# Performance work log

Measured on AMD Instinct MI355X. Metric: run time of the kernel, lower is better.

The kernel has to match this reference:

```python
import jax, jax.numpy as jnp
import numpy as np

EMBED_DIM = 1024
NUM_HEADS = 16
HEAD_DIM = EMBED_DIM // NUM_HEADS
B, S = 4, 2048


def setup_inputs() -> dict:
    key = jax.random.key(0)
    ks = jax.random.split(key, 9)
    scale = 1.0 / np.sqrt(EMBED_DIM)
    x = jax.random.normal(ks[0], (B, S, EMBED_DIM), dtype=jnp.float32)
    Wq = jax.random.normal(ks[1], (EMBED_DIM, EMBED_DIM), dtype=jnp.float32) * scale
    Wk = jax.random.normal(ks[2], (EMBED_DIM, EMBED_DIM), dtype=jnp.float32) * scale
    Wv = jax.random.normal(ks[3], (EMBED_DIM, EMBED_DIM), dtype=jnp.float32) * scale
    Wo = jax.random.normal(ks[4], (EMBED_DIM, EMBED_DIM), dtype=jnp.float32) * scale
    bq = jnp.zeros((EMBED_DIM,), jnp.float32)
    bk = jnp.zeros((EMBED_DIM,), jnp.float32)
    bv = jnp.zeros((EMBED_DIM,), jnp.float32)
    bo = jnp.zeros((EMBED_DIM,), jnp.float32)
    return {"x": x, "Wq": Wq, "bq": bq, "Wk": Wk, "bk": bk, "Wv": Wv, "bv": bv, "Wo": Wo, "bo": bo}


def _split_heads(t):
    # [B,S,E] -> [B,H,S,D]
    b, s, _ = t.shape
    return t.reshape(b, s, NUM_HEADS, HEAD_DIM).transpose(0, 2, 1, 3)


def reference(x, Wq, bq, Wk, bk, Wv, bv, Wo, bo):
    q = _split_heads(x @ Wq + bq)
    k = _split_heads(x @ Wk + bk)
    v = _split_heads(x @ Wv + bv)
    scale = 1.0 / jnp.sqrt(jnp.asarray(HEAD_DIM, x.dtype))
    scores = jnp.einsum('bhqd,bhkd->bhqk', q, k) * scale  # [B,H,S,S]
    weights = jax.nn.softmax(scores, axis=-1)
    attn = jnp.einsum('bhqk,bhkd->bhqd', weights, v)  # [B,H,S,D]
    b, h, s, d = attn.shape
    concat = attn.transpose(0, 2, 1, 3).reshape(b, s, h * d)
    return concat @ Wo + bo
```

## Files before the change

### kernel.cpp

```cpp
#include <hip/hip_runtime.h>
#include <hip/hip_bf16.h>

typedef unsigned short u16;
typedef __attribute__((ext_vector_type(8))) short bf16x8;
typedef __attribute__((ext_vector_type(4))) float f32x4;
typedef __attribute__((ext_vector_type(4))) unsigned int u32x4;

#define EMB 1024
#define SEQ 2048
#define NH 16
#define HD 64

#define OFF_WT   0u
#define OFF_WOT  3145728u
#define OFF_Q    4194304u
#define OFF_K    12582912u
#define OFF_VT   20971520u
#define OFF_OC   29360128u

#define QSCALE 0.1803368801111f

__device__ __forceinline__ u16 f2bf(float f) {
    unsigned int x; __builtin_memcpy(&x, &f, 4);
    unsigned int r = x + 0x7fffu + ((x >> 16) & 1u);
    return (u16)(r >> 16);
}

#if defined(__has_builtin) && __has_builtin(__builtin_amdgcn_cvt_pk_bf16_f32)
typedef __attribute__((ext_vector_type(2))) __bf16 bfv2;
__device__ __forceinline__ unsigned int pkbf(float a, float b) {
    bfv2 v = __builtin_amdgcn_cvt_pk_bf16_f32(a, b);
    unsigned int u; __builtin_memcpy(&u, &v, 4); return u;
}
#else
__device__ __forceinline__ unsigned int pkbf(float a, float b) {
    return (unsigned)f2bf(a) | ((unsigned)f2bf(b) << 16);
}
#endif

#if defined(__has_builtin) && __has_builtin(__builtin_amdgcn_exp2f)
__device__ __forceinline__ float exp2fast(float x) { return __builtin_amdgcn_exp2f(x); }
#else
__device__ __forceinline__ float exp2fast(float x) { return __builtin_exp2f(x); }
#endif

__device__ __forceinline__ void gld_lds16(const void* gsrc, void* ldst) {
    void* g = const_cast<void*>(gsrc);
    __builtin_amdgcn_global_load_lds((__attribute__((address_space(1))) void*)g,
                                     (__attribute__((address_space(3))) void*)ldst,
                                     16, 0, 0);
}

__global__ __launch_bounds__(256) void convert_x(
    const float* __restrict__ x, u16* __restrict__ xb)
{
    int i = (blockIdx.x * 256 + threadIdx.x) * 4;
    float4 v = *(const float4*)&x[i];
    uint2 o = { pkbf(v.x, v.y), pkbf(v.z, v.w) };
    *(uint2*)&xb[i] = o;
}

__global__ __launch_bounds__(256) void transpose_w(
    const float* __restrict__ W0, const float* __restrict__ W1,
    const float* __restrict__ W2, const float* __restrict__ W3,
    u16* __restrict__ ws)
{
    __shared__ u16 tile[64 * 65];
    const float* src = blockIdx.z == 0 ? W0 : blockIdx.z == 1 ? W1 : blockIdx.z == 2 ? W2 : W3;
    u16* dst = ws + (blockIdx.z < 3 ? (unsigned)blockIdx.z * 1048576u : OFF_WOT);
    const int k0 = blockIdx.x * 64, n0 = blockIdx.y * 64;
    const int t = threadIdx.x;
    #pragma unroll
    for (int i = 0; i < 16; i++) {
        int idx = i * 256 + t; int r = idx >> 6, c = idx & 63;
        tile[c * 65 + r] = f2bf(src[(k0 + r) * EMB + n0 + c]);
    }
    __syncthreads();
    #pragma unroll
    for (int i = 0; i < 16; i++) {
        int idx = i * 256 + t; int r = idx >> 6, c = idx & 63;
        dst[(n0 + r) * EMB + k0 + c] = tile[r * 65 + c];
    }
}

__global__ __launch_bounds__(256) void gemm_qkv(
    const u16* __restrict__ X, const u16* __restrict__ WT,
    const float* __restrict__ bq, const float* __restrict__ bk, const float* __restrict__ bv,
    u16* __restrict__ Qt, u16* __restrict__ Ko, u16* __restrict__ Vt)
{
    __shared__ u16 Al[128 * 32];
    __shared__ u16 Bl[128 * 32];
    const int t = threadIdx.x, lane = t & 63, w = t >> 6;
    const int quad = lane >> 4, l15 = lane & 15;
    const int wr = w >> 1, wc = w & 1;
    const int m0 = blockIdx.x * 128, n0 = blockIdx.y * 128;
    const f32x4 fzero = {0.f, 0.f, 0.f, 0.f};

    f32x4 acc[4][4];
    #pragma unroll
    for (int i = 0; i < 4; i++)
        #pragma unroll
        for (int j = 0; j < 4; j++) acc[i][j] = fzero;

    for (int kt = 0; kt < 32; ++kt) {
        #pragma unroll
        for (int r = 0; r < 2; r++) {
            int g = r * 256 + t; int row = g >> 2, cw = g & 3;
            int sc = (cw ^ ((row >> 1) & 3)) * 8;
            gld_lds16(X  + (size_t)(m0 + row) * EMB + kt * 32 + sc, &Al[g * 8]);
            gld_lds16(WT + (size_t)(n0 + row) * EMB + kt * 32 + sc, &Bl[g * 8]);
        }
        __syncthreads();
        bf16x8 af[4], bfr[4];
        #pragma unroll
        for (int i = 0; i < 4; i++) {
            int rowA = wr * 64 + i * 16 + l15;
            af[i] = *(const bf16x8*)&Al[rowA * 32 + ((quad ^ ((rowA >> 1) & 3)) * 8)];
        }
        #pragma unroll
        for (int j = 0; j < 4; j++) {
            int rowB = wc * 64 + j * 16 + l15;
            bfr[j] = *(const bf16x8*)&Bl[rowB * 32 + ((quad ^ ((rowB >> 1) & 3)) * 8)];
        }
        #pragma unroll
        for (int i = 0; i < 4; i++)
            #pragma unroll
            for (int j = 0; j < 4; j++)
                acc[i][j] = __builtin_amdgcn_mfma_f32_16x16x32_bf16(af[i], bfr[j], acc[i][j], 0, 0, 0);
        __syncthreads();
    }

    const int seg = n0 >> 10;
    const float* bias = seg == 0 ? bq : (seg == 1 ? bk : bv);
    #pragma unroll
    for (int j = 0; j < 4; j++) {
        int n = n0 + wc * 64 + j * 16 + l15;
        int nn = n & 1023;
        float bvl = bias[nn];
        int h = nn >> 6, d = nn & 63;
        #pragma unroll
        for (int i = 0; i < 4; i++) {
            int m = m0 + wr * 64 + i * 16 + quad * 4;
            int b = m >> 11, s = m & 2047;
            if (seg == 0) {
                uint2 pp = { pkbf((acc[i][j][0] + bvl) * QSCALE, (acc[i][j][1] + bvl) * QSCALE),
                             pkbf((acc[i][j][2] + bvl) * QSCALE, (acc[i][j][3] + bvl) * QSCALE) };
                *(uint2*)&Qt[(size_t)((b * NH + h) * HD + d) * SEQ + s] = pp;
            } else if (seg == 2) {
                uint2 pp = { pkbf(acc[i][j][0] + bvl, acc[i][j][1] + bvl),
                             pkbf(acc[i][j][2] + bvl, acc[i][j][3] + bvl) };
                *(uint2*)&Vt[(size_t)((b * NH + h) * HD + d) * SEQ + s] = pp;
            } else {
                size_t base = (size_t)((b * NH + h) * SEQ + s) * HD + d;
                #pragma unroll
                for (int r = 0; r < 4; r++) Ko[base + (size_t)r * HD] = f2bf(acc[i][j][r] + bvl);
            }
        }
    }
}

__global__ __launch_bounds__(256, 2) void flash_attn(
    const u16* __restrict__ Q, const u16* __restrict__ K,
    const u16* __restrict__ VT, u16* __restrict__ Oc)
{
    __shared__ u16 Kl[2][64 * 64];
    __shared__ u16 Vl[2][64 * 64];
    const int t = threadIdx.x, lane = t & 63, w = t >> 6;
    const int quad = lane >> 4, l15 = lane & 15;
    const int a7 = l15 & 7;

    const int lin = blockIdx.x;
    const int xcd = lin & 7, slot = lin >> 3;
    const int bh = xcd * 8 + (slot >> 3);
    const int qx = slot & 7;
    const int b = bh >> 4, h = bh & 15;
    const int q0 = qx * 256 + w * 64;

    const u16* Qtb = Q + (size_t)bh * HD * SEQ;
    const u16* Kb  = K + (size_t)bh * SEQ * HD;
    const u16* Vb  = VT + (size_t)bh * HD * SEQ;
    const f32x4 fzero = {0.f, 0.f, 0.f, 0.f};

    const int kf0 = l15 * 64 + ((quad ^ a7) * 8);
    const int kf1 = l15 * 64 + (((4 + quad) ^ a7) * 8);

    bf16x8 ones;
    #pragma unroll
    for (int j = 0; j < 8; j++) ones[j] = (short)0x3F80;

    bf16x8 qf[4][2];
    #pragma unroll
    for (int i = 0; i < 4; i++)
        #pragma unroll
        for (int c = 0; c < 2; c++)
            #pragma unroll
            for (int j = 0; j < 8; j++)
                qf[i][c][j] = (short)Qtb[(size_t)(c * 32 + quad * 8 + j) * SEQ + q0 + i * 16 + l15];

    f32x4 oacc[4][4];
    f32x4 oextra[4];
    #pragma unroll
    for (int i = 0; i < 4; i++) {
        oextra[i] = fzero;
        #pragma unroll
        for (int f = 0; f < 4; f++) oacc[i][f] = fzero;
    }

    auto stage = [&](int kt, int bsel) {
        #pragma unroll
        for (int r = 0; r < 2; r++) {
            int g = r * 256 + t, row = g >> 3, cw = g & 7;
            int swz = (cw ^ (row & 7)) * 8;
            gld_lds16(Kb + (size_t)kt * 64 * HD + row * HD + swz, &Kl[bsel][g * 8]);
            gld_lds16(Vb + (size_t)row * SEQ + kt * 64 + swz, &Vl[bsel][g * 8]);
        }
    };

    stage(0, 0);
    asm volatile("s_waitcnt vmcnt(0) lgkmcnt(0)" ::: "memory");
    __builtin_amdgcn_s_barrier();
    __builtin_amdgcn_sched_barrier(0);

    int cur = 0;
    for (int kt = 0; kt < 32; ++kt) {
        if (kt < 31) stage(kt + 1, cur ^ 1);

        const u16* kbuf = &Kl[cur][0];
        const u16* vbuf = &Vl[cur][0];
        bf16x8 ak[2][4], av[2][4];
        #pragma unroll
        for (int f = 0; f < 4; f++) {
            ak[0][f] = *(const bf16x8*)(kbuf + kf0 + f * 1024);
            ak[1][f] = *(const bf16x8*)(kbuf + kf1 + f * 1024);
            av[0][f] = *(const bf16x8*)(vbuf + kf0 + f * 1024);
            av[1][f] = *(const bf16x8*)(vbuf + kf1 + f * 1024);
        }

        #pragma unroll
        for (int i = 0; i < 4; i++) {
            f32x4 sf[4];
            #pragma unroll
            for (int f = 0; f < 4; f++) sf[f] = fzero;
            __builtin_amdgcn_s_setprio(1);
            #pragma unroll
            for (int c = 0; c < 2; c++)
                #pragma unroll
                for (int f = 0; f < 4; f++)
                    sf[f] = __builtin_amdgcn_mfma_f32_16x16x32_bf16(ak[c][f], qf[i][c], sf[f], 0, 0, 0);
            __builtin_amdgcn_s_setprio(0);

            unsigned int pa[4][2];
            #pragma unroll
            for (int f = 0; f < 4; f++) {
                pa[f][0] = pkbf(exp2fast(sf[f][0]), exp2fast(sf[f][1]));
                pa[f][1] = pkbf(exp2fast(sf[f][2]), exp2fast(sf[f][3]));
            }

            unsigned int z0 = pa[0][0], w0 = pa[1][0];
            asm("v_permlane32_swap_b32 %0, %1" : "+v"(z0), "+v"(w0));
            asm("v_permlane16_swap_b32 %0, %1" : "+v"(z0), "+v"(w0));
            unsigned int z1 = pa[0][1], w1 = pa[1][1];
            asm("v_permlane32_swap_b32 %0, %1" : "+v"(z1), "+v"(w1));
            asm("v_permlane16_swap_b32 %0, %1" : "+v"(z1), "+v"(w1));
            unsigned int z2 = pa[2][0], w2 = pa[3][0];
            asm("v_permlane32_swap_b32 %0, %1" : "+v"(z2), "+v"(w2));
            asm("v_permlane16_swap_b32 %0, %1" : "+v"(z2), "+v"(w2));
            unsigned int z3 = pa[2][1], w3 = pa[3][1];
            asm("v_permlane32_swap_b32 %0, %1" : "+v"(z3), "+v"(w3));
            asm("v_permlane16_swap_b32 %0, %1" : "+v"(z3), "+v"(w3));

            bf16x8 bp0, bp1;
            { u32x4 u = {z0, z1, w0, w1}; __builtin_memcpy(&bp0, &u, 16); }
            { u32x4 u = {z2, z3, w2, w3}; __builtin_memcpy(&bp1, &u, 16); }

            __builtin_amdgcn_s_setprio(1);
            #pragma unroll
            for (int f = 0; f < 4; f++) {
                oacc[i][f] = __builtin_amdgcn_mfma_f32_16x16x32_bf16(av[0][f], bp0, oacc[i][f], 0, 0, 0);
                oacc[i][f] = __builtin_amdgcn_mfma_f32_16x16x32_bf16(av[1][f], bp1, oacc[i][f], 0, 0, 0);
            }
            oextra[i] = __builtin_amdgcn_mfma_f32_16x16x32_bf16(ones, bp0, oextra[i], 0, 0, 0);
            oextra[i] = __builtin_amdgcn_mfma_f32_16x16x32_bf16(ones, bp1, oextra[i], 0, 0, 0);
            __builtin_amdgcn_s_setprio(0);
        }

        if (kt < 31) {
            asm volatile("s_waitcnt vmcnt(0) lgkmcnt(0)" ::: "memory");
            __builtin_amdgcn_s_barrier();
            __builtin_amdgcn_sched_barrier(0);
        }
        cur ^= 1;
    }

    #pragma unroll
    for (int i = 0; i < 4; i++) {
        float inv = 1.0f / oextra[i][0];
        int s = q0 + i * 16 + l15;
        size_t base = ((size_t)(b * SEQ + s) * NH + h) * HD;
        #pragma unroll
        for (int f = 0; f < 4; f++) {
            uint2 o = { pkbf(oacc[i][f][0] * inv, oacc[i][f][1] * inv),
                        pkbf(oacc[i][f][2] * inv, oacc[i][f][3] * inv) };
            *(uint2*)&Oc[base + f * 16 + quad * 4] = o;
        }
    }
}

__global__ __launch_bounds__(256) void gemm_out(
    const u16* __restrict__ A, const u16* __restrict__ WT,
    const float* __restrict__ bo, float* __restrict__ out)
{
    __shared__ u16 Al[128 * 32];
    __shared__ u16 Bl[128 * 32];
    const int t = threadIdx.x, lane = t & 63, w = t >> 6;
    const int quad = lane >> 4, l15 = lane & 15;
    const int wr = w >> 1, wc = w & 1;
    const int m0 = blockIdx.x * 128, n0 = blockIdx.y * 128;
    const f32x4 fzero = {0.f, 0.f, 0.f, 0.f};

    f32x4 acc[4][4];
    #pragma unroll
    for (int i = 0; i < 4; i++)
        #pragma unroll
        for (int j = 0; j < 4; j++) acc[i][j] = fzero;

    for (int kt = 0; kt < 32; ++kt) {
        #pragma unroll
        for (int r = 0; r < 2; r++) {
            int g = r * 256 + t; int row = g >> 2, cw = g & 3;
            int sc = (cw ^ ((row >> 1) & 3)) * 8;
            gld_lds16(A  + (size_t)(m0 + row) * EMB + kt * 32 + sc, &Al[g * 8]);
            gld_lds16(WT + (size_t)(n0 + row) * EMB + kt * 32 + sc, &Bl[g * 8]);
        }
        __syncthreads();
        bf16x8 af[4], bfr[4];
        #pragma unroll
        for (int i = 0; i < 4; i++) {
            int rowA = wr * 64 + i * 16 + l15;
            af[i] = *(const bf16x8*)&Al[rowA * 32 + ((quad ^ ((rowA >> 1) & 3)) * 8)];
        }
        #pragma unroll
        for (int j = 0; j < 4; j++) {
            int rowB = wc * 64 + j * 16 + l15;
            bfr[j] = *(const bf16x8*)&Bl[rowB * 32 + ((quad ^ ((rowB >> 1) & 3)) * 8)];
        }
        #pragma unroll
        for (int i = 0; i < 4; i++)
            #pragma unroll
            for (int j = 0; j < 4; j++)
                acc[i][j] = __builtin_amdgcn_mfma_f32_16x16x32_bf16(af[i], bfr[j], acc[i][j], 0, 0, 0);
        __syncthreads();
    }

    #pragma unroll
    for (int j = 0; j < 4; j++) {
        int n = n0 + wc * 64 + j * 16 + l15;
        float bvl = bo[n];
        #pragma unroll
        for (int i = 0; i < 4; i++) {
            int m = m0 + wr * 64 + i * 16 + quad * 4;
            #pragma unroll
            for (int r = 0; r < 4; r++)
                out[(size_t)(m + r) * EMB + n] = acc[i][j][r] + bvl;
        }
    }
}

extern "C" void kernel_launch(void* const* d_in, const int* in_sizes, int n_in,
                              void* d_out, int out_size, void* d_ws, size_t ws_size,
                              hipStream_t stream)
{
    (void)in_sizes; (void)n_in; (void)out_size; (void)ws_size;
    const float* x  = (const float*)d_in[0];
    const float* Wq = (const float*)d_in[1];
    const float* bq = (const float*)d_in[2];
    const float* Wk = (const float*)d_in[3];
    const float* bk = (const float*)d_in[4];
    const float* Wv = (const float*)d_in[5];
    const float* bv = (const float*)d_in[6];
    const float* Wo = (const float*)d_in[7];
    const float* bo = (const float*)d_in[8];
    u16* ws = (u16*)d_ws;
    u16* Xb = (u16*)d_out;

    convert_x<<<dim3(8192), 256, 0, stream>>>(x, Xb);
    transpose_w<<<dim3(16, 16, 4), 256, 0, stream>>>(Wq, Wk, Wv, Wo, ws);
    gemm_qkv<<<dim3(64, 24), 256, 0, stream>>>(Xb, ws + OFF_WT, bq, bk, bv,
                                               ws + OFF_Q, ws + OFF_K, ws + OFF_VT);
    flash_attn<<<dim3(512), 256, 0, stream>>>(ws + OFF_Q, ws + OFF_K,
                                              ws + OFF_VT, ws + OFF_OC);
    gemm_out<<<dim3(64, 8), 256, 0, stream>>>(ws + OFF_OC, ws + OFF_WOT, bo, (float*)d_out);
}
```

Measured before the change: 293.4 us.

## Deepen flash-attention K/V staging to four buffers and drop permlane swaps via K row permutation

Flash attention now stages K/V tiles into a four-slot LDS ring with a prefetch distance of two, waiting on partial vmcnt instead of draining all loads each iteration. This is meant to overlap global loads with MFMA work more deeply. K rows are loaded in a permuted order so that the exp'd score fragments land directly in the layout the PV MFMA expects, which removes the permlane32/16 swap instructions. LDS use doubles, which may reduce occupancy. The permutation must match the operand layout exactly or the results will be wrong.

```diff
diff --git a/kernel.cpp b/kernel.cpp
--- a/kernel.cpp
+++ b/kernel.cpp
@@ -163,8 +163,8 @@
     const u16* __restrict__ Q, const u16* __restrict__ K,
     const u16* __restrict__ VT, u16* __restrict__ Oc)
 {
-    __shared__ u16 Kl[2][64 * 64];
-    __shared__ u16 Vl[2][64 * 64];
+    __shared__ u16 Kl[4][64 * 64];
+    __shared__ u16 Vl[4][64 * 64];
     const int t = threadIdx.x, lane = t & 63, w = t >> 6;
     const int quad = lane >> 4, l15 = lane & 15;
     const int a7 = l15 & 7;
@@ -211,22 +211,15 @@
         for (int r = 0; r < 2; r++) {
             int g = r * 256 + t, row = g >> 3, cw = g & 7;
             int swz = (cw ^ (row & 7)) * 8;
-            gld_lds16(Kb + (size_t)kt * 64 * HD + row * HD + swz, &Kl[bsel][g * 8]);
+            int gk = ((row & 2) << 4) | (((row >> 2) & 3) << 3) | ((row >> 4) << 1) | (row & 1);
+            gld_lds16(Kb + (size_t)kt * 64 * HD + gk * HD + swz, &Kl[bsel][g * 8]);
             gld_lds16(Vb + (size_t)row * SEQ + kt * 64 + swz, &Vl[bsel][g * 8]);
         }
     };
 
-    stage(0, 0);
-    asm volatile("s_waitcnt vmcnt(0) lgkmcnt(0)" ::: "memory");
-    __builtin_amdgcn_s_barrier();
-    __builtin_amdgcn_sched_barrier(0);
-
-    int cur = 0;
-    for (int kt = 0; kt < 32; ++kt) {
-        if (kt < 31) stage(kt + 1, cur ^ 1);
-
-        const u16* kbuf = &Kl[cur][0];
-        const u16* vbuf = &Vl[cur][0];
+    auto compute = [&](int kt) {
+        const u16* kbuf = &Kl[kt & 3][0];
+        const u16* vbuf = &Vl[kt & 3][0];
         bf16x8 ak[2][4], av[2][4];
         #pragma unroll
         for (int f = 0; f < 4; f++) {
@@ -239,39 +232,23 @@
         #pragma unroll
         for (int i = 0; i < 4; i++) {
             f32x4 sf[4];
-            #pragma unroll
-            for (int f = 0; f < 4; f++) sf[f] = fzero;
             __builtin_amdgcn_s_setprio(1);
             #pragma unroll
-            for (int c = 0; c < 2; c++)
-                #pragma unroll
-                for (int f = 0; f < 4; f++)
-                    sf[f] = __builtin_amdgcn_mfma_f32_16x16x32_bf16(ak[c][f], qf[i][c], sf[f], 0, 0, 0);
+            for (int f = 0; f < 4; f++) {
+                sf[f] = __builtin_amdgcn_mfma_f32_16x16x32_bf16(ak[0][f], qf[i][0], fzero, 0, 0, 0);
+                sf[f] = __builtin_amdgcn_mfma_f32_16x16x32_bf16(ak[1][f], qf[i][1], sf[f], 0, 0, 0);
+            }
             __builtin_amdgcn_s_setprio(0);
 
-            unsigned int pa[4][2];
+            unsigned int w0[4], w1[4];
             #pragma unroll
             for (int f = 0; f < 4; f++) {
-                pa[f][0] = pkbf(exp2fast(sf[f][0]), exp2fast(sf[f][1]));
-                pa[f][1] = pkbf(exp2fast(sf[f][2]), exp2fast(sf[f][3]));
+                w0[f] = pkbf(exp2fast(sf[f][0]), exp2fast(sf[f][1]));
+                w1[f] = pkbf(exp2fast(sf[f][2]), exp2fast(sf[f][3]));
             }
-
-            unsigned int z0 = pa[0][0], w0 = pa[1][0];
-            asm("v_permlane32_swap_b32 %0, %1" : "+v"(z0), "+v"(w0));
-            asm("v_permlane16_swap_b32 %0, %1" : "+v"(z0), "+v"(w0));
-            unsigned int z1 = pa[0][1], w1 = pa[1][1];
-            asm("v_permlane32_swap_b32 %0, %1" : "+v"(z1), "+v"(w1));
-            asm("v_permlane16_swap_b32 %0, %1" : "+v"(z1), "+v"(w1));
-            unsigned int z2 = pa[2][0], w2 = pa[3][0];
-            asm("v_permlane32_swap_b32 %0, %1" : "+v"(z2), "+v"(w2));
-            asm("v_permlane16_swap_b32 %0, %1" : "+v"(z2), "+v"(w2));
-            unsigned int z3 = pa[2][1], w3 = pa[3][1];
-            asm("v_permlane32_swap_b32 %0, %1" : "+v"(z3), "+v"(w3));
-            asm("v_permlane16_swap_b32 %0, %1" : "+v"(z3), "+v"(w3));
-
             bf16x8 bp0, bp1;
-            { u32x4 u = {z0, z1, w0, w1}; __builtin_memcpy(&bp0, &u, 16); }
-            { u32x4 u = {z2, z3, w2, w3}; __builtin_memcpy(&bp1, &u, 16); }
+            { u32x4 u = {w0[0], w0[1], w0[2], w0[3]}; __builtin_memcpy(&bp0, &u, 16); }
+            { u32x4 u = {w1[0], w1[1], w1[2], w1[3]}; __builtin_memcpy(&bp1, &u, 16); }
 
             __builtin_amdgcn_s_setprio(1);
             #pragma unroll
@@ -283,14 +260,23 @@
             oextra[i] = __builtin_amdgcn_mfma_f32_16x16x32_bf16(ones, bp1, oextra[i], 0, 0, 0);
             __builtin_amdgcn_s_setprio(0);
         }
-
-        if (kt < 31) {
-            asm volatile("s_waitcnt vmcnt(0) lgkmcnt(0)" ::: "memory");
-            __builtin_amdgcn_s_barrier();
-            __builtin_amdgcn_sched_barrier(0);
-        }
-        cur ^= 1;
-    }
+    };
+
+    stage(0, 0);
+    stage(1, 1);
+
+    for (int kt = 0; kt < 30; ++kt) {
+        stage(kt + 2, (kt + 2) & 3);
+        asm volatile("s_waitcnt vmcnt(16)" ::: "memory");
+        __builtin_amdgcn_s_barrier();
+        compute(kt);
+    }
+    asm volatile("s_waitcnt vmcnt(8)" ::: "memory");
+    __builtin_amdgcn_s_barrier();
+    compute(30);
+    asm volatile("s_waitcnt vmcnt(0)" ::: "memory");
+    __builtin_amdgcn_s_barrier();
+    compute(31);
 
     #pragma unroll
     for (int i = 0; i < 4; i++) {
```

Result: faster. 279.1 us (-4.9%).
